# Optimization experiments

Hardware: AMD Instinct MI355X
Metric: run time of the kernel (lower is better)

Reference implementation:

```python
import jax, jax.numpy as jnp
import numpy as np

N, F, R, E, L = 100000, 128, 4, 1600000, 2


def setup_inputs() -> dict:
    key = jax.random.key(0)
    k1, k2, k3, k4, k5 = jax.random.split(key, 5)
    scale = 1.0 / np.sqrt(F)
    x = jax.random.normal(k1, (N, F), dtype=jnp.float32)
    edge_index = jax.random.randint(k2, (2, E), 0, N, dtype=jnp.int64)
    edge_type = jax.random.randint(k3, (E,), 0, R, dtype=jnp.int64)
    weights = jax.random.normal(k4, (L, R, F, F), dtype=jnp.float32) * scale
    roots = jax.random.normal(k5, (L, F, F), dtype=jnp.float32) * scale
    biases = jnp.zeros((L, F), dtype=jnp.float32)
    return {"x": x, "edge_index": edge_index, "edge_type": edge_type,
            "weights": weights, "roots": roots, "biases": biases}


def _rgcn_layer(x, weight, root, bias, src, dst, etype):
    # weight: [R, F, F]. Transform all nodes by all relation weights: [R, N, F]
    xw = jnp.einsum('nf,rfo->rno', x, weight)
    msgs = xw[etype, src]                       # [E, F] gather per edge
    seg = dst * R + etype                       # combined (node, relation) segment id
    sums = jax.ops.segment_sum(msgs, seg, num_segments=N * R)
    cnt = jax.ops.segment_sum(jnp.ones((msgs.shape[0],), msgs.dtype), seg,
                              num_segments=N * R)
    mean = sums / jnp.maximum(cnt, 1.0)[:, None]  # mean aggregation per relation
    agg = mean.reshape(N, R, F).sum(axis=1)       # sum over relations: [N, F]
    return agg + x @ root + bias


def reference(x, edge_index, edge_type, weights, roots, biases):
    src, dst = edge_index[0], edge_index[1]
    for l in range(L):
        x = _rgcn_layer(x, weights[l], roots[l], biases[l], src, dst, edge_type)
        x = jax.nn.relu(x)  # dropout is identity at eval
    return x
```

## Files before the change

### kernel.cpp

```cpp
#include <hip/hip_runtime.h>
#include <hip/hip_bf16.h>

#define N_NODES 100000
#define FDIM 128
#define RREL 4
#define NEDGE 1600000
#define NSEG (N_NODES * RREL)
#define KB_TOT 20
#define BSW_PER_LAYER (KB_TOT * 8 * 64 * 8)
#define BIN_SHIFT 10
#define BIN_SEGS 1024
#define NBINS ((NSEG + BIN_SEGS - 1) / BIN_SEGS)
#define BIN_CAP 5120
#define EPB 2048

typedef __attribute__((ext_vector_type(8))) short bfrag;
typedef __attribute__((ext_vector_type(4))) float ffrag;

__device__ __forceinline__ unsigned short f2bf(float f) {
    unsigned u = __float_as_uint(f);
    u += 0x7fffu + ((u >> 16) & 1u);
    return (unsigned short)(u >> 16);
}
__device__ __forceinline__ float bf_lo(unsigned u) { return __uint_as_float(u << 16); }
__device__ __forceinline__ float bf_hi(unsigned u) { return __uint_as_float(u & 0xffff0000u); }

__global__ __launch_bounds__(256) void cast_x(
    const float* __restrict__ x, unsigned short* __restrict__ xb)
{
    int i = blockIdx.x * 256 + threadIdx.x;
    float4 v = ((const float4*)x)[i];
    ushort4 o = { f2bf(v.x), f2bf(v.y), f2bf(v.z), f2bf(v.w) };
    ((ushort4*)xb)[i] = o;
}

__global__ __launch_bounds__(256) void prep_weights(
    const float* __restrict__ W,
    const float* __restrict__ root,
    unsigned short* __restrict__ Bsw,
    int* __restrict__ binCursor)
{
    int idx = blockIdx.x * 256 + threadIdx.x;
    if (blockIdx.x < 2) {
        int t = blockIdx.x * 256 + threadIdx.x;
        if (t < NBINS) binCursor[t] = 0;
    }
    int layer = idx / BSW_PER_LAYER;
    int rem = idx % BSW_PER_LAYER;
    int kb = rem / 4096;
    int rem2 = rem % 4096;
    int ct = rem2 / 512;
    int rem3 = rem2 % 512;
    int lane = rem3 / 8;
    int j = rem3 % 8;
    int k = kb * 32 + (lane >> 4) * 8 + j;
    int n = ct * 16 + (lane & 15);
    float v;
    if (k < 512) v = W[(size_t)layer * 4 * 128 * 128 + (size_t)k * 128 + n];
    else         v = root[(size_t)layer * 128 * 128 + (size_t)(k - 512) * 128 + n];
    Bsw[idx] = f2bf(v);
}

__global__ __launch_bounds__(256) void bin_scatter(
    const int* __restrict__ src, const int* __restrict__ dst,
    const int* __restrict__ et, int* __restrict__ binCursor,
    uint2* __restrict__ pairs)
{
    __shared__ int hist[NBINS];
    __shared__ int base[NBINS];
    int tid = threadIdx.x;
    for (int b = tid; b < NBINS; b += 256) hist[b] = 0;
    __syncthreads();
    int e0 = blockIdx.x * EPB;
    int segr[EPB / 256], srcr[EPB / 256];
    #pragma unroll
    for (int i = 0; i < EPB / 256; ++i) {
        int e = e0 + i * 256 + tid;
        if (e < NEDGE) {
            segr[i] = dst[e] * RREL + et[e];
            srcr[i] = src[e];
            atomicAdd(&hist[segr[i] >> BIN_SHIFT], 1);
        } else segr[i] = -1;
    }
    __syncthreads();
    for (int b = tid; b < NBINS; b += 256) {
        int h = hist[b];
        base[b] = h ? atomicAdd(&binCursor[b], h) : 0;
        hist[b] = 0;
    }
    __syncthreads();
    #pragma unroll
    for (int i = 0; i < EPB / 256; ++i) {
        if (segr[i] >= 0) {
            int b = segr[i] >> BIN_SHIFT;
            int li = atomicAdd(&hist[b], 1);
            pairs[(size_t)b * BIN_CAP + base[b] + li] =
                make_uint2((unsigned)srcr[i], (unsigned)segr[i]);
        }
    }
}

__global__ __launch_bounds__(1024) void bin_fill(
    const uint2* __restrict__ pairs, const int* __restrict__ binCursor,
    int* __restrict__ esrc, int* __restrict__ counts, int* __restrict__ cursor)
{
    __shared__ int hist[BIN_SEGS];
    __shared__ int cur[BIN_SEGS];
    __shared__ int waveSums[16];
    int b = blockIdx.x;
    int tid = threadIdx.x;
    int seg0 = b << BIN_SHIFT;
    int cnt = binCursor[b];
    size_t pb = (size_t)b * BIN_CAP;
    hist[tid] = 0;
    __syncthreads();
    for (int i = tid; i < cnt; i += 1024)
        atomicAdd(&hist[pairs[pb + i].y - (unsigned)seg0], 1);
    __syncthreads();
    int v = hist[tid];
    int lane = tid & 63, wv = tid >> 6;
    int inc = v;
    #pragma unroll
    for (int d = 1; d < 64; d <<= 1) {
        int o = __shfl_up(inc, d, 64);
        if (lane >= d) inc += o;
    }
    if (lane == 63) waveSums[wv] = inc;
    __syncthreads();
    int wbase = 0;
    for (int w = 0; w < wv; ++w) wbase += waveSums[w];
    int glob = (int)pb + wbase + inc - v;
    int sg = seg0 + tid;
    if (sg < NSEG) { counts[sg] = v; cursor[sg] = glob; }
    cur[tid] = glob;
    __syncthreads();
    for (int i = tid; i < cnt; i += 1024) {
        uint2 p = pairs[pb + i];
        int pos = atomicAdd(&cur[p.y - (unsigned)seg0], 1);
        esrc[pos] = (int)p.x;
    }
}

__global__ __launch_bounds__(256) void rgcn_aggregate(
    const unsigned short* __restrict__ xb, const int* __restrict__ esrc,
    const int* __restrict__ cursor, const int* __restrict__ counts,
    unsigned short* __restrict__ meanb)
{
    int sub = threadIdx.x >> 4;
    int lane16 = threadIdx.x & 15;
    int seg = blockIdx.x * 16 + sub;
    int j = cursor[seg];
    int c = counts[seg];
    int end = j + c;
    float acc[8] = {};
    for (; j + 1 < end; j += 2) {
        int s0 = esrc[j], s1 = esrc[j + 1];
        uint4 u0 = ((const uint4*)(xb + (size_t)s0 * FDIM))[lane16];
        uint4 u1 = ((const uint4*)(xb + (size_t)s1 * FDIM))[lane16];
        acc[0] += bf_lo(u0.x) + bf_lo(u1.x);
        acc[1] += bf_hi(u0.x) + bf_hi(u1.x);
        acc[2] += bf_lo(u0.y) + bf_lo(u1.y);
        acc[3] += bf_hi(u0.y) + bf_hi(u1.y);
        acc[4] += bf_lo(u0.z) + bf_lo(u1.z);
        acc[5] += bf_hi(u0.z) + bf_hi(u1.z);
        acc[6] += bf_lo(u0.w) + bf_lo(u1.w);
        acc[7] += bf_hi(u0.w) + bf_hi(u1.w);
    }
    if (j < end) {
        int sv = esrc[j];
        uint4 u = ((const uint4*)(xb + (size_t)sv * FDIM))[lane16];
        acc[0] += bf_lo(u.x); acc[1] += bf_hi(u.x);
        acc[2] += bf_lo(u.y); acc[3] += bf_hi(u.y);
        acc[4] += bf_lo(u.z); acc[5] += bf_hi(u.z);
        acc[6] += bf_lo(u.w); acc[7] += bf_hi(u.w);
    }
    float inv = 1.0f / fmaxf((float)c, 1.0f);
    uint4 o;
    o.x = (unsigned)f2bf(acc[0] * inv) | ((unsigned)f2bf(acc[1] * inv) << 16);
    o.y = (unsigned)f2bf(acc[2] * inv) | ((unsigned)f2bf(acc[3] * inv) << 16);
    o.z = (unsigned)f2bf(acc[4] * inv) | ((unsigned)f2bf(acc[5] * inv) << 16);
    o.w = (unsigned)f2bf(acc[6] * inv) | ((unsigned)f2bf(acc[7] * inv) << 16);
    ((uint4*)(meanb + (size_t)seg * FDIM))[lane16] = o;
}

__global__ __launch_bounds__(256, 2) void rgcn_transform(
    const unsigned short* __restrict__ xb,
    const unsigned short* __restrict__ meanb,
    const unsigned short* __restrict__ Bsw,
    const float* __restrict__ bias,
    float* __restrict__ out,
    unsigned short* __restrict__ xbn,
    const int writeF32)
{
    __shared__ __align__(16) unsigned char Bsm[2][8192];

    int tid = threadIdx.x;
    int wave = tid >> 6, lane = tid & 63;
    int quad = lane >> 4, rlo = lane & 15;
    int n0 = blockIdx.x * 128 + wave * 32;
    int r0 = n0 + rlo;
    int r1 = n0 + 16 + rlo;
    int r0c = min(r0, N_NODES - 1);
    int r1c = min(r1, N_NODES - 1);

    const bfrag* m0 = (const bfrag*)(meanb + (size_t)r0c * 512) + quad;
    const bfrag* m1 = (const bfrag*)(meanb + (size_t)r1c * 512) + quad;
    const bfrag* x0 = (const bfrag*)(xb + (size_t)r0c * FDIM) + quad;
    const bfrag* x1 = (const bfrag*)(xb + (size_t)r1c * FDIM) + quad;

    const uint4* gB = (const uint4*)Bsw;
    #define STAGE_B(kb, buf) do { \
        uint4* _s = (uint4*)Bsm[buf]; \
        const uint4* _g = gB + (kb) * 512; \
        _s[tid] = _g[tid]; \
        _s[tid + 256] = _g[tid + 256]; \
    } while (0)

    #define AFRAG(row, kb) ((kb) < 16 ? row##_m[(kb) * 4] : row##_x[((kb) - 16) * 4])
    const bfrag* r0_m = m0; const bfrag* r0_x = x0;
    const bfrag* r1_m = m1; const bfrag* r1_x = x1;

    ffrag acc[2][8] = {};

    STAGE_B(0, 0);
    bfrag a0p0 = AFRAG(r0, 0), a1p0 = AFRAG(r1, 0);
    bfrag a0p1 = AFRAG(r0, 1), a1p1 = AFRAG(r1, 1);
    __syncthreads();

    #pragma unroll
    for (int kb = 0; kb < KB_TOT; ++kb) {
        int cur = kb & 1;
        if (kb + 1 < KB_TOT) STAGE_B(kb + 1, cur ^ 1);

        bfrag a0 = cur ? a0p1 : a0p0;
        bfrag a1 = cur ? a1p1 : a1p0;
        if (kb + 2 < KB_TOT) {
            if (cur) { a0p1 = AFRAG(r0, kb + 2); a1p1 = AFRAG(r1, kb + 2); }
            else     { a0p0 = AFRAG(r0, kb + 2); a1p0 = AFRAG(r1, kb + 2); }
        }

        #pragma unroll
        for (int ct = 0; ct < 8; ++ct) {
            bfrag b = *(const bfrag*)&Bsm[cur][ct * 1024 + lane * 16];
            acc[0][ct] = __builtin_amdgcn_mfma_f32_16x16x32_bf16(a0, b, acc[0][ct], 0, 0, 0);
            acc[1][ct] = __builtin_amdgcn_mfma_f32_16x16x32_bf16(a1, b, acc[1][ct], 0, 0, 0);
        }
        __syncthreads();
    }
    #undef STAGE_B
    #undef AFRAG

    float bcol[8];
    #pragma unroll
    for (int ct = 0; ct < 8; ++ct) bcol[ct] = bias[ct * 16 + rlo];

    #pragma unroll
    for (int rt = 0; rt < 2; ++rt) {
        int rbase = n0 + rt * 16 + quad * 4;
        #pragma unroll
        for (int i = 0; i < 4; ++i) {
            int r = rbase + i;
            if (r < N_NODES) {
                #pragma unroll
                for (int ct = 0; ct < 8; ++ct) {
                    float v = fmaxf(acc[rt][ct][i] + bcol[ct], 0.0f);
                    int col = ct * 16 + rlo;
                    if (writeF32) out[(size_t)r * FDIM + col] = v;
                    else          xbn[(size_t)r * FDIM + col] = f2bf(v);
                }
            }
        }
    }
}

extern "C" void kernel_launch(void* const* d_in, const int* in_sizes, int n_in,
                              void* d_out, int out_size, void* d_ws, size_t ws_size,
                              hipStream_t stream) {
    const float* x        = (const float*)d_in[0];
    const int* edge_index = (const int*)d_in[1];
    const int* edge_type  = (const int*)d_in[2];
    const float* weights  = (const float*)d_in[3];
    const float* roots    = (const float*)d_in[4];
    const float* biases   = (const float*)d_in[5];
    float* out = (float*)d_out;

    unsigned short* meanb = (unsigned short*)d_ws;
    uint2* pairs = (uint2*)d_ws;
    unsigned short* xb0   = meanb + (size_t)NSEG * FDIM;
    unsigned short* xb1   = xb0 + (size_t)N_NODES * FDIM;
    unsigned short* Bsw   = xb1 + (size_t)N_NODES * FDIM;
    int* esrc   = (int*)(Bsw + 2 * BSW_PER_LAYER);
    int* counts = esrc + (size_t)NBINS * BIN_CAP;
    int* cursor = counts + NSEG;
    int* binCursor = cursor + NSEG;

    const int* src = edge_index;
    const int* dst = edge_index + NEDGE;

    cast_x<<<(N_NODES * FDIM / 4) / 256, 256, 0, stream>>>(x, xb0);
    prep_weights<<<2 * BSW_PER_LAYER / 256, 256, 0, stream>>>(weights, roots, Bsw,
                                                              binCursor);
    bin_scatter<<<(NEDGE + EPB - 1) / EPB, 256, 0, stream>>>(src, dst, edge_type,
                                                             binCursor, pairs);
    bin_fill<<<NBINS, 1024, 0, stream>>>(pairs, binCursor, esrc, counts, cursor);

    const int tgrid = (N_NODES + 127) / 128;

    rgcn_aggregate<<<NSEG / 16, 256, 0, stream>>>(xb0, esrc, cursor, counts, meanb);
    rgcn_transform<<<tgrid, 256, 0, stream>>>(xb0, meanb, Bsw, biases, out, xb1, 0);
    rgcn_aggregate<<<NSEG / 16, 256, 0, stream>>>(xb1, esrc, cursor, counts, meanb);
    rgcn_transform<<<tgrid, 256, 0, stream>>>(xb1, meanb, Bsw + BSW_PER_LAYER,
                                              biases + FDIM, out, xb0, 1);
}
```

Before: 386.8 us.

## Fuse prep kernels, pack edge pairs, unroll gather, drop LDS B staging

Merges the x cast and weight prep into one launch, and packs each binned edge into a single 32-bit word (src shifted above a 10-bit local segment id), which halves the pair traffic between bin_scatter and bin_fill. The aggregate gather is unrolled to four rows per iteration with 32-bit offset math to raise memory-level parallelism. The transform kernel stops staging B through double-buffered LDS with barriers and reads B fragments straight from global/L2. The direct loads remove sync overhead but may raise global load latency on the MFMA path.

```diff
diff --git a/kernel.cpp b/kernel.cpp
--- a/kernel.cpp
+++ b/kernel.cpp
@@ -13,6 +13,8 @@
 #define NBINS ((NSEG + BIN_SEGS - 1) / BIN_SEGS)
 #define BIN_CAP 5120
 #define EPB 2048
+#define CAST_NB ((N_NODES * FDIM / 4) / 256)
+#define PREP_NB (2 * BSW_PER_LAYER / 256)
 
 typedef __attribute__((ext_vector_type(8))) short bfrag;
 typedef __attribute__((ext_vector_type(4))) float ffrag;
@@ -25,24 +27,24 @@
 __device__ __forceinline__ float bf_lo(unsigned u) { return __uint_as_float(u << 16); }
 __device__ __forceinline__ float bf_hi(unsigned u) { return __uint_as_float(u & 0xffff0000u); }
 
-__global__ __launch_bounds__(256) void cast_x(
-    const float* __restrict__ x, unsigned short* __restrict__ xb)
-{
-    int i = blockIdx.x * 256 + threadIdx.x;
-    float4 v = ((const float4*)x)[i];
-    ushort4 o = { f2bf(v.x), f2bf(v.y), f2bf(v.z), f2bf(v.w) };
-    ((ushort4*)xb)[i] = o;
-}
-
-__global__ __launch_bounds__(256) void prep_weights(
+__global__ __launch_bounds__(256) void prep(
+    const float* __restrict__ x, unsigned short* __restrict__ xb,
     const float* __restrict__ W,
     const float* __restrict__ root,
     unsigned short* __restrict__ Bsw,
     int* __restrict__ binCursor)
 {
-    int idx = blockIdx.x * 256 + threadIdx.x;
-    if (blockIdx.x < 2) {
-        int t = blockIdx.x * 256 + threadIdx.x;
+    if (blockIdx.x < CAST_NB) {
+        int i = blockIdx.x * 256 + threadIdx.x;
+        float4 v = ((const float4*)x)[i];
+        ushort4 o = { f2bf(v.x), f2bf(v.y), f2bf(v.z), f2bf(v.w) };
+        ((ushort4*)xb)[i] = o;
+        return;
+    }
+    int wb = blockIdx.x - CAST_NB;
+    int idx = wb * 256 + threadIdx.x;
+    if (wb < 2) {
+        int t = wb * 256 + threadIdx.x;
         if (t < NBINS) binCursor[t] = 0;
     }
     int layer = idx / BSW_PER_LAYER;
@@ -64,7 +66,7 @@
 __global__ __launch_bounds__(256) void bin_scatter(
     const int* __restrict__ src, const int* __restrict__ dst,
     const int* __restrict__ et, int* __restrict__ binCursor,
-    uint2* __restrict__ pairs)
+    unsigned* __restrict__ pairs)
 {
     __shared__ int hist[NBINS];
     __shared__ int base[NBINS];
@@ -72,15 +74,17 @@
     for (int b = tid; b < NBINS; b += 256) hist[b] = 0;
     __syncthreads();
     int e0 = blockIdx.x * EPB;
-    int segr[EPB / 256], srcr[EPB / 256];
+    int binr[EPB / 256];
+    unsigned pkr[EPB / 256];
     #pragma unroll
     for (int i = 0; i < EPB / 256; ++i) {
         int e = e0 + i * 256 + tid;
         if (e < NEDGE) {
-            segr[i] = dst[e] * RREL + et[e];
-            srcr[i] = src[e];
-            atomicAdd(&hist[segr[i] >> BIN_SHIFT], 1);
-        } else segr[i] = -1;
+            int seg = dst[e] * RREL + et[e];
+            binr[i] = seg >> BIN_SHIFT;
+            pkr[i] = ((unsigned)src[e] << BIN_SHIFT) | (unsigned)(seg & (BIN_SEGS - 1));
+            atomicAdd(&hist[binr[i]], 1);
+        } else binr[i] = -1;
     }
     __syncthreads();
     for (int b = tid; b < NBINS; b += 256) {
@@ -91,17 +95,16 @@
     __syncthreads();
     #pragma unroll
     for (int i = 0; i < EPB / 256; ++i) {
-        if (segr[i] >= 0) {
-            int b = segr[i] >> BIN_SHIFT;
+        if (binr[i] >= 0) {
+            int b = binr[i];
             int li = atomicAdd(&hist[b], 1);
-            pairs[(size_t)b * BIN_CAP + base[b] + li] =
-                make_uint2((unsigned)srcr[i], (unsigned)segr[i]);
+            pairs[(size_t)b * BIN_CAP + base[b] + li] = pkr[i];
         }
     }
 }
 
 __global__ __launch_bounds__(1024) void bin_fill(
-    const uint2* __restrict__ pairs, const int* __restrict__ binCursor,
+    const unsigned* __restrict__ pairs, const int* __restrict__ binCursor,
     int* __restrict__ esrc, int* __restrict__ counts, int* __restrict__ cursor)
 {
     __shared__ int hist[BIN_SEGS];
@@ -115,7 +118,7 @@
     hist[tid] = 0;
     __syncthreads();
     for (int i = tid; i < cnt; i += 1024)
-        atomicAdd(&hist[pairs[pb + i].y - (unsigned)seg0], 1);
+        atomicAdd(&hist[pairs[pb + i] & (BIN_SEGS - 1)], 1);
     __syncthreads();
     int v = hist[tid];
     int lane = tid & 63, wv = tid >> 6;
@@ -135,10 +138,21 @@
     cur[tid] = glob;
     __syncthreads();
     for (int i = tid; i < cnt; i += 1024) {
-        uint2 p = pairs[pb + i];
-        int pos = atomicAdd(&cur[p.y - (unsigned)seg0], 1);
-        esrc[pos] = (int)p.x;
-    }
+        unsigned p = pairs[pb + i];
+        int pos = atomicAdd(&cur[p & (BIN_SEGS - 1)], 1);
+        esrc[pos] = (int)(p >> BIN_SHIFT);
+    }
+}
+
+__device__ __forceinline__ uint4 ldrow(const unsigned short* xb, int s, int lane16) {
+    unsigned off = (unsigned)s * (FDIM * 2) + (unsigned)lane16 * 16u;
+    return *(const uint4*)((const char*)xb + off);
+}
+__device__ __forceinline__ void acc_add(float* acc, uint4 u) {
+    acc[0] += bf_lo(u.x); acc[1] += bf_hi(u.x);
+    acc[2] += bf_lo(u.y); acc[3] += bf_hi(u.y);
+    acc[4] += bf_lo(u.z); acc[5] += bf_hi(u.z);
+    acc[6] += bf_lo(u.w); acc[7] += bf_hi(u.w);
 }
 
 __global__ __launch_bounds__(256) void rgcn_aggregate(
@@ -153,26 +167,18 @@
     int c = counts[seg];
     int end = j + c;
     float acc[8] = {};
-    for (; j + 1 < end; j += 2) {
-        int s0 = esrc[j], s1 = esrc[j + 1];
-        uint4 u0 = ((const uint4*)(xb + (size_t)s0 * FDIM))[lane16];
-        uint4 u1 = ((const uint4*)(xb + (size_t)s1 * FDIM))[lane16];
-        acc[0] += bf_lo(u0.x) + bf_lo(u1.x);
-        acc[1] += bf_hi(u0.x) + bf_hi(u1.x);
-        acc[2] += bf_lo(u0.y) + bf_lo(u1.y);
-        acc[3] += bf_hi(u0.y) + bf_hi(u1.y);
-        acc[4] += bf_lo(u0.z) + bf_lo(u1.z);
-        acc[5] += bf_hi(u0.z) + bf_hi(u1.z);
-        acc[6] += bf_lo(u0.w) + bf_lo(u1.w);
-        acc[7] += bf_hi(u0.w) + bf_hi(u1.w);
-    }
-    if (j < end) {
+    for (; j + 3 < end; j += 4) {
+        int s0 = esrc[j], s1 = esrc[j + 1], s2 = esrc[j + 2], s3 = esrc[j + 3];
+        uint4 u0 = ldrow(xb, s0, lane16);
+        uint4 u1 = ldrow(xb, s1, lane16);
+        uint4 u2 = ldrow(xb, s2, lane16);
+        uint4 u3 = ldrow(xb, s3, lane16);
+        acc_add(acc, u0); acc_add(acc, u1); acc_add(acc, u2); acc_add(acc, u3);
+    }
+    for (; j < end; ++j) {
         int sv = esrc[j];
-        uint4 u = ((const uint4*)(xb + (size_t)sv * FDIM))[lane16];
-        acc[0] += bf_lo(u.x); acc[1] += bf_hi(u.x);
-        acc[2] += bf_lo(u.y); acc[3] += bf_hi(u.y);
-        acc[4] += bf_lo(u.z); acc[5] += bf_hi(u.z);
-        acc[6] += bf_lo(u.w); acc[7] += bf_hi(u.w);
+        uint4 u = ldrow(xb, sv, lane16);
+        acc_add(acc, u);
     }
     float inv = 1.0f / fmaxf((float)c, 1.0f);
     uint4 o;
@@ -192,63 +198,43 @@
     unsigned short* __restrict__ xbn,
     const int writeF32)
 {
-    __shared__ __align__(16) unsigned char Bsm[2][8192];
-
     int tid = threadIdx.x;
     int wave = tid >> 6, lane = tid & 63;
     int quad = lane >> 4, rlo = lane & 15;
     int n0 = blockIdx.x * 128 + wave * 32;
-    int r0 = n0 + rlo;
-    int r1 = n0 + 16 + rlo;
-    int r0c = min(r0, N_NODES - 1);
-    int r1c = min(r1, N_NODES - 1);
+    int r0c = min(n0 + rlo, N_NODES - 1);
+    int r1c = min(n0 + 16 + rlo, N_NODES - 1);
 
     const bfrag* m0 = (const bfrag*)(meanb + (size_t)r0c * 512) + quad;
     const bfrag* m1 = (const bfrag*)(meanb + (size_t)r1c * 512) + quad;
     const bfrag* x0 = (const bfrag*)(xb + (size_t)r0c * FDIM) + quad;
     const bfrag* x1 = (const bfrag*)(xb + (size_t)r1c * FDIM) + quad;
-
-    const uint4* gB = (const uint4*)Bsw;
-    #define STAGE_B(kb, buf) do { \
-        uint4* _s = (uint4*)Bsm[buf]; \
-        const uint4* _g = gB + (kb) * 512; \
-        _s[tid] = _g[tid]; \
-        _s[tid + 256] = _g[tid + 256]; \
-    } while (0)
-
-    #define AFRAG(row, kb) ((kb) < 16 ? row##_m[(kb) * 4] : row##_x[((kb) - 16) * 4])
-    const bfrag* r0_m = m0; const bfrag* r0_x = x0;
-    const bfrag* r1_m = m1; const bfrag* r1_x = x1;
+    const bfrag* bl = (const bfrag*)Bsw + lane;
 
     ffrag acc[2][8] = {};
 
-    STAGE_B(0, 0);
-    bfrag a0p0 = AFRAG(r0, 0), a1p0 = AFRAG(r1, 0);
-    bfrag a0p1 = AFRAG(r0, 1), a1p1 = AFRAG(r1, 1);
-    __syncthreads();
-
-    #pragma unroll
-    for (int kb = 0; kb < KB_TOT; ++kb) {
-        int cur = kb & 1;
-        if (kb + 1 < KB_TOT) STAGE_B(kb + 1, cur ^ 1);
-
-        bfrag a0 = cur ? a0p1 : a0p0;
-        bfrag a1 = cur ? a1p1 : a1p0;
-        if (kb + 2 < KB_TOT) {
-            if (cur) { a0p1 = AFRAG(r0, kb + 2); a1p1 = AFRAG(r1, kb + 2); }
-            else     { a0p0 = AFRAG(r0, kb + 2); a1p0 = AFRAG(r1, kb + 2); }
-        }
-
+    #pragma unroll 2
+    for (int kb = 0; kb < 16; ++kb) {
+        bfrag a0 = m0[kb * 4];
+        bfrag a1 = m1[kb * 4];
         #pragma unroll
         for (int ct = 0; ct < 8; ++ct) {
-            bfrag b = *(const bfrag*)&Bsm[cur][ct * 1024 + lane * 16];
+            bfrag b = bl[(kb * 8 + ct) * 64];
             acc[0][ct] = __builtin_amdgcn_mfma_f32_16x16x32_bf16(a0, b, acc[0][ct], 0, 0, 0);
             acc[1][ct] = __builtin_amdgcn_mfma_f32_16x16x32_bf16(a1, b, acc[1][ct], 0, 0, 0);
         }
-        __syncthreads();
-    }
-    #undef STAGE_B
-    #undef AFRAG
+    }
+    #pragma unroll 2
+    for (int kb = 16; kb < 20; ++kb) {
+        bfrag a0 = x0[(kb - 16) * 4];
+        bfrag a1 = x1[(kb - 16) * 4];
+        #pragma unroll
+        for (int ct = 0; ct < 8; ++ct) {
+            bfrag b = bl[(kb * 8 + ct) * 64];
+            acc[0][ct] = __builtin_amdgcn_mfma_f32_16x16x32_bf16(a0, b, acc[0][ct], 0, 0, 0);
+            acc[1][ct] = __builtin_amdgcn_mfma_f32_16x16x32_bf16(a1, b, acc[1][ct], 0, 0, 0);
+        }
+    }
 
     float bcol[8];
     #pragma unroll
@@ -285,7 +271,7 @@
     float* out = (float*)d_out;
 
     unsigned short* meanb = (unsigned short*)d_ws;
-    uint2* pairs = (uint2*)d_ws;
+    unsigned* pairs = (unsigned*)d_ws;
     unsigned short* xb0   = meanb + (size_t)NSEG * FDIM;
     unsigned short* xb1   = xb0 + (size_t)N_NODES * FDIM;
     unsigned short* Bsw   = xb1 + (size_t)N_NODES * FDIM;
@@ -297,9 +283,8 @@
     const int* src = edge_index;
     const int* dst = edge_index + NEDGE;
 
-    cast_x<<<(N_NODES * FDIM / 4) / 256, 256, 0, stream>>>(x, xb0);
-    prep_weights<<<2 * BSW_PER_LAYER / 256, 256, 0, stream>>>(weights, roots, Bsw,
-                                                              binCursor);
+    prep<<<CAST_NB + PREP_NB, 256, 0, stream>>>(x, xb0, weights, roots, Bsw,
+                                                binCursor);
     bin_scatter<<<(NEDGE + EPB - 1) / EPB, 256, 0, stream>>>(src, dst, edge_type,
                                                              binCursor, pairs);
     bin_fill<<<NBINS, 1024, 0, stream>>>(pairs, binCursor, esrc, counts, cursor);
```

After: 392.6 us. No clear change (+1.5%).
